# Kernel tuning notes

Measured on AMD Instinct MI355X. Metric: run time of the kernel, lower is better.

Reference implementation:

```python
import jax, jax.numpy as jnp
import numpy as np

B, K, D = 8, 2048, 1024

def setup_inputs() -> dict:
    key = jax.random.key(0)
    k1, k2 = jax.random.split(key)
    x = jax.random.normal(k1, (B, K, D), dtype=jnp.float32)
    W = jax.random.normal(k2, (K, K), dtype=jnp.float32) * 0.02  # dt_proj weight [out=K, in=K]
    b = jnp.zeros((K,), dtype=jnp.float32)                        # dt_proj bias
    return {"x": x, "W": W, "b": b}

def _scan_combine(c1, c2):
    # compose affine maps s -> a*s + u; (a1,u1) then (a2,u2)
    a1, u1 = c1
    a2, u2 = c2
    return (a2 * a1, a2 * u1 + u2)

def reference(x, W, b):
    # lam[b,t,d] = sigmoid( sum_k x[b,k,d] * W[t,k] + b[t] )
    # (dt_proj is a Linear over the TIME axis after permute(0,2,1))
    lam = jax.nn.sigmoid(jnp.einsum('bkd,tk->btd', x, W) + b[None, :, None])
    # s_t = lam_t * s_{t-1} + (1 - lam_t) * x_t, s_0 = 0  -> associative scan over time
    _, ys = jax.lax.associative_scan(_scan_combine, (lam, (1.0 - lam) * x), axis=1)
    return ys
```

## Files before the change

### kernel.cpp

```cpp
#include <hip/hip_runtime.h>
#include <hip/hip_bf16.h>
#include <stdint.h>

#define B_ 8
#define K_ 2048
#define D_ 1024
#define NC 32
#define TC (K_ / NC)

typedef float v4f __attribute__((ext_vector_type(4)));
typedef short v8s __attribute__((ext_vector_type(8)));

__device__ __forceinline__ unsigned short f2bf(float f) {
    __hip_bfloat16 h = __float2bfloat16(f);
    return *reinterpret_cast<unsigned short*>(&h);
}

__device__ __forceinline__ void async_ld16(const void* g, void* l) {
    __builtin_amdgcn_global_load_lds(
        (__attribute__((address_space(1))) void*)(void*)g,
        (__attribute__((address_space(3))) void*)l,
        16, 0, 0);
}

__global__ void conv_all(const float* __restrict__ W, unsigned short* __restrict__ Wb,
                         const float* __restrict__ x, unsigned short* __restrict__ xT) {
    if (blockIdx.x < 4096) {
        int i = (blockIdx.x * 256 + threadIdx.x) * 4;
        float4 v = *(const float4*)(W + i);
        ushort4 o;
        o.x = f2bf(v.x); o.y = f2bf(v.y); o.z = f2bf(v.z); o.w = f2bf(v.w);
        *(ushort4*)(Wb + i) = o;
        return;
    }
    const int t = blockIdx.x - 4096;
    const int k0 = (t & 31) * 64, d0 = ((t >> 5) & 15) * 64, bb = t >> 9;
    __shared__ unsigned short tile[64][68];
    const int tid = threadIdx.x;
    const int tx = tid & 15, ty = tid >> 4;
    const float* xp = x + (size_t)bb * K_ * D_;
#pragma unroll
    for (int r = 0; r < 4; r++) {
        int row = ty + r * 16;
        float4 v = *(const float4*)(xp + (size_t)(k0 + row) * D_ + d0 + tx * 4);
        tile[row][tx * 4 + 0] = f2bf(v.x);
        tile[row][tx * 4 + 1] = f2bf(v.y);
        tile[row][tx * 4 + 2] = f2bf(v.z);
        tile[row][tx * 4 + 3] = f2bf(v.w);
    }
    __syncthreads();
    unsigned short* op = xT + (size_t)bb * D_ * K_;
#pragma unroll
    for (int r = 0; r < 4; r++) {
        int dcol = ty + r * 16;
        ushort4 u;
        u.x = tile[tx * 4 + 0][dcol];
        u.y = tile[tx * 4 + 1][dcol];
        u.z = tile[tx * 4 + 2][dcol];
        u.w = tile[tx * 4 + 3][dcol];
        *(ushort4*)(op + (size_t)(d0 + dcol) * K_ + k0 + tx * 4) = u;
    }
}

__launch_bounds__(512, 2)
__global__ void gemm_sig(const unsigned short* __restrict__ Wb,
                         const unsigned short* __restrict__ xT,
                         const float* __restrict__ bias,
                         const float* __restrict__ xf,
                         float* __restrict__ lam,
                         float* __restrict__ Ac,
                         float* __restrict__ Uc,
                         int fuse) {
    __shared__ __align__(16) unsigned short smem_all[2][4][256 * 32];

    const int bid = blockIdx.x;
    const int lid = (bid & 7) * 32 + (bid >> 3);
    const int bb = lid >> 5;
    const int tM = (lid >> 2) & 7;
    const int tN = lid & 3;

    const int tid = threadIdx.x;
    const int w = tid >> 6;
    const int lane = tid & 63;
    const int wm = w >> 2;
    const int wn = w & 3;
    const int quad = lane >> 4;
    const int l16 = lane & 15;

    const unsigned short* Ag = Wb + (size_t)(tM * 256) * K_;
    const unsigned short* Bg = xT + (size_t)bb * D_ * K_ + (size_t)(tN * 256) * K_;

    const int srow = lane >> 2;
    const int sgk8 = ((lane & 3) ^ ((lane >> 3) & 3)) * 8;

    const int frg = (quad ^ ((l16 >> 1) & 3)) * 8;
    const int aoff = (wm * 128 + l16) * 32 + frg;
    const int boff = (wn * 64 + l16) * 32 + frg;

    v4f acc[8][4];
#pragma unroll
    for (int i = 0; i < 8; i++)
#pragma unroll
        for (int j = 0; j < 4; j++) acc[i][j] = (v4f)0.f;

#define STAGE_A_(hh)                                                                        \
    do {                                                                                    \
        const int slot_ = (hh) & 3; const int ko_ = (hh) * 32;                              \
        async_ld16(Ag + (size_t)(w * 16 + srow) * K_ + ko_ + sgk8,                          \
                   &smem_all[0][slot_][w * 512]);                                           \
        async_ld16(Ag + (size_t)((8 + w) * 16 + srow) * K_ + ko_ + sgk8,                    \
                   &smem_all[0][slot_][(8 + w) * 512]);                                     \
    } while (0)
#define STAGE_B_(hh)                                                                        \
    do {                                                                                    \
        const int slot_ = (hh) & 3; const int ko_ = (hh) * 32;                              \
        async_ld16(Bg + (size_t)(w * 16 + srow) * K_ + ko_ + sgk8,                          \
                   &smem_all[1][slot_][w * 512]);                                           \
        async_ld16(Bg + (size_t)((8 + w) * 16 + srow) * K_ + ko_ + sgk8,                    \
                   &smem_all[1][slot_][(8 + w) * 512]);                                     \
    } while (0)

    v8s af[8], bf[2];

#define HALF_(hh, DO_STAGE, VM_)                                                            \
    do {                                                                                    \
        const int s_ = (hh) & 3;                                                            \
        const unsigned short* As_ = &smem_all[0][s_][0];                                    \
        const unsigned short* Bs_ = &smem_all[1][s_][0];                                    \
                                                                   \
        _Pragma("unroll")                                                                   \
        for (int i = 0; i < 8; i++) af[i] = *(const v8s*)(&As_[aoff + i * 512]);            \
        bf[0] = *(const v8s*)(&Bs_[boff]);                                                  \
        bf[1] = *(const v8s*)(&Bs_[boff + 512]);                                            \
        if (DO_STAGE) STAGE_A_((hh) + 3);                                                   \
        asm volatile("s_barrier" ::: "memory");                                             \
        asm volatile("s_waitcnt lgkmcnt(0)");                                               \
        __builtin_amdgcn_sched_barrier(0);                                                  \
        __builtin_amdgcn_s_setprio(1);                                                      \
        _Pragma("unroll")                                                                   \
        for (int i = 0; i < 8; i++) {                                                       \
            acc[i][0] = __builtin_amdgcn_mfma_f32_16x16x32_bf16(af[i], bf[0], acc[i][0], 0, 0, 0); \
            acc[i][1] = __builtin_amdgcn_mfma_f32_16x16x32_bf16(af[i], bf[1], acc[i][1], 0, 0, 0); \
        }                                                                                   \
        __builtin_amdgcn_s_setprio(0);                                                      \
        asm volatile("s_barrier" ::: "memory");                                             \
                                                                   \
        bf[0] = *(const v8s*)(&Bs_[boff + 2 * 512]);                                        \
        bf[1] = *(const v8s*)(&Bs_[boff + 3 * 512]);                                        \
        if (DO_STAGE) STAGE_B_((hh) + 3);                                                   \
        asm volatile("s_barrier" ::: "memory");                                             \
        asm volatile("s_waitcnt lgkmcnt(0)");                                               \
        __builtin_amdgcn_sched_barrier(0);                                                  \
        __builtin_amdgcn_s_setprio(1);                                                      \
        _Pragma("unroll")                                                                   \
        for (int i = 0; i < 8; i++) {                                                       \
            acc[i][2] = __builtin_amdgcn_mfma_f32_16x16x32_bf16(af[i], bf[0], acc[i][2], 0, 0, 0); \
            acc[i][3] = __builtin_amdgcn_mfma_f32_16x16x32_bf16(af[i], bf[1], acc[i][3], 0, 0, 0); \
        }                                                                                   \
        __builtin_amdgcn_s_setprio(0);                                                      \
        VM_;                                                                                \
        asm volatile("s_barrier" ::: "memory");                                             \
    } while (0)

    STAGE_A_(0); STAGE_B_(0);
    STAGE_A_(1); STAGE_B_(1);
    STAGE_A_(2); STAGE_B_(2);
    asm volatile("s_waitcnt vmcnt(8)");
    asm volatile("s_barrier" ::: "memory");

    const int H = K_ / 32;
    for (int h = 0; h < H - 3; ++h)
        HALF_(h, 1, asm volatile("s_waitcnt vmcnt(8)"));
    HALF_(H - 3, 0, asm volatile("s_waitcnt vmcnt(4)"));
    HALF_(H - 2, 0, asm volatile("s_waitcnt vmcnt(0)"));
    HALF_(H - 1, 0, (void)0);
#undef HALF_
#undef STAGE_A_
#undef STAGE_B_


    float* out = lam + (size_t)bb * K_ * D_;
    const int dg = tN * 256 + wn * 64;

    if (fuse) {
        float* Swp = (float*)smem_all + w * 4096;
        const int swzw = quad * 16;
#pragma unroll
        for (int cg = 0; cg < 2; cg++) {
            const int c = tM * 4 + wm * 2 + cg;
            const int t0 = c * 64;
#pragma unroll
            for (int ii = 0; ii < 4; ii++) {
                int i = cg * 4 + ii;
                int rowb = t0 + ii * 16 + quad * 4;
                int Rb = ii * 16 + quad * 4;
#pragma unroll
                for (int r = 0; r < 4; r++) {
                    float bt = bias[rowb + r];
#pragma unroll
                    for (int j = 0; j < 4; j++) {
                        int colc = j * 16 + l16;
                        float v = acc[i][j][r] + bt;
                        float sg = 1.f / (1.f + __expf(-v));
                        out[(size_t)(rowb + r) * D_ + dg + colc] = sg;
                        Swp[(Rb + r) * 64 + (colc ^ swzw)] = sg;
                    }
                }
            }
            asm volatile("s_waitcnt lgkmcnt(0)");
            __builtin_amdgcn_sched_barrier(0);
            const float* xg = xf + ((size_t)bb * K_ + t0) * D_ + dg + lane;
            float A = 1.f, U = 0.f;
#pragma unroll 8
            for (int tt = 0; tt < 64; tt++) {
                float l = Swp[tt * 64 + (lane ^ (((tt >> 2) & 3) * 16))];
                float xv = xg[(size_t)tt * D_];
                A *= l;
                U = l * U + (1.f - l) * xv;
            }
            size_t oi = ((size_t)bb * NC + c) * D_ + dg + lane;
            Ac[oi] = A;
            Uc[oi] = U;
            __builtin_amdgcn_sched_barrier(0);
        }
    } else {
#pragma unroll
        for (int i = 0; i < 8; i++) {
            int rowb = tM * 256 + wm * 128 + i * 16 + quad * 4;
#pragma unroll
            for (int r = 0; r < 4; r++) {
                float bt = bias[rowb + r];
#pragma unroll
                for (int j = 0; j < 4; j++) {
                    int col = tN * 256 + wn * 64 + j * 16 + l16;
                    float v = acc[i][j][r] + bt;
                    out[(size_t)(rowb + r) * D_ + col] = 1.f / (1.f + __expf(-v));
                }
            }
        }
    }
}

__global__ void scan_pass1(const float* __restrict__ lam, const float* __restrict__ x,
                           float* __restrict__ Ac, float* __restrict__ Uc) {
    int id = blockIdx.x * 256 + threadIdx.x;
    int d2 = (id & 511) * 2;
    int c = (id >> 9) & (NC - 1);
    int bb = id >> 14;
    const float* lp = lam + ((size_t)bb * K_ + (size_t)c * TC) * D_ + d2;
    const float* xp = x   + ((size_t)bb * K_ + (size_t)c * TC) * D_ + d2;
    float2 A = make_float2(1.f, 1.f), U = make_float2(0.f, 0.f);
#pragma unroll 8
    for (int t = 0; t < TC; t++) {
        float2 l  = *(const float2*)(lp + (size_t)t * D_);
        float2 xv = *(const float2*)(xp + (size_t)t * D_);
        A.x *= l.x; A.y *= l.y;
        U.x = l.x * U.x + (1.f - l.x) * xv.x;
        U.y = l.y * U.y + (1.f - l.y) * xv.y;
    }
    size_t oi = ((size_t)bb * NC + c) * D_ + d2;
    *(float2*)(Ac + oi) = A;
    *(float2*)(Uc + oi) = U;
}

__launch_bounds__(256)
__global__ void scan_pass3(const float* __restrict__ x,
                           const float* __restrict__ Ac, const float* __restrict__ Uc,
                           float* __restrict__ lamout) {
    int id = blockIdx.x * 256 + threadIdx.x;
    int d = (id & 511) * 2;
    int c = (id >> 9) & (NC - 1);
    int bb = id >> 14;
    float2 s = make_float2(0.f, 0.f);
    for (int j = 0; j < c; j++) {
        size_t ji = ((size_t)bb * NC + j) * D_ + d;
        float2 A = *(const float2*)(Ac + ji);
        float2 U = *(const float2*)(Uc + ji);
        s.x = A.x * s.x + U.x;
        s.y = A.y * s.y + U.y;
    }
    float* lp = lamout + ((size_t)bb * K_ + (size_t)c * TC) * D_ + d;
    const float* xp = x + ((size_t)bb * K_ + (size_t)c * TC) * D_ + d;
#pragma unroll 8
    for (int t = 0; t < TC; t++) {
        float2 l  = *(const float2*)(lp + (size_t)t * D_);
        float2 xv = *(const float2*)(xp + (size_t)t * D_);
        s.x = l.x * s.x + (1.f - l.x) * xv.x;
        s.y = l.y * s.y + (1.f - l.y) * xv.y;
        __builtin_nontemporal_store(s.x, lp + (size_t)t * D_);
        __builtin_nontemporal_store(s.y, lp + (size_t)t * D_ + 1);
    }
}

extern "C" void kernel_launch(void* const* d_in, const int* in_sizes, int n_in,
                              void* d_out, int out_size, void* d_ws, size_t ws_size,
                              hipStream_t stream) {
    const float* x    = (const float*)d_in[0];
    const float* W    = (const float*)d_in[1];
    const float* bias = (const float*)d_in[2];
    float* out = (float*)d_out;
    char* ws = (char*)d_ws;

    unsigned short* xT = (unsigned short*)ws;
    unsigned short* Wb = (unsigned short*)(ws + 33554432);

    const int fuse = (ws_size >= 44040192u) ? 1 : 0;
    float* Ac, * Uc;
    if (fuse) {
        Ac = (float*)(ws + 41943040);
        Uc = (float*)(ws + 41943040 + 1048576);
    } else {
        Ac = (float*)(ws + 33554432);
        Uc = (float*)(ws + 33554432 + 1048576);
    }

    conv_all<<<dim3(8192), 256, 0, stream>>>(W, Wb, x, xT);
    gemm_sig<<<dim3(256), dim3(512), 0, stream>>>(Wb, xT, bias, x, out, Ac, Uc, fuse);
    if (!fuse)
        scan_pass1<<<dim3(B_ * NC * D_ / 2 / 256), 256, 0, stream>>>(out, x, Ac, Uc);
    scan_pass3<<<dim3(B_ * NC * D_ / 2 / 256), 256, 0, stream>>>(x, Ac, Uc, out);
}
```

Measured before the change: 237.2 us.

## Prefetch next A fragments into registers during second MFMA half

Adds register double-buffering of the A operand fragments. The next stage's A tile is loaded from LDS into a second register set while the current stage's MFMAs run. The explicit lgkmcnt(0) waits and sched_barriers are removed so the compiler can overlap LDS reads with matrix math. Global-load waits are tightened to vmcnt(4) because the next slot must land one stage earlier. This trades more VGPR pressure, which may cut occupancy, for hiding LDS latency.

Result: slower. 243.0 us (+2.4%).

```diff
diff --git a/kernel.cpp b/kernel.cpp
--- a/kernel.cpp
+++ b/kernel.cpp
@@ -120,22 +120,17 @@
                    &smem_all[1][slot_][(8 + w) * 512]);                                     \
     } while (0)
 
-    v8s af[8], bf[2];
-
-#define HALF_(hh, DO_STAGE, VM_)                                                            \
+    v8s af[8], afn[8], bf[2];
+
+#define HALF_(hh, DO_STG, DO_AFN, VM_)                                                      \
     do {                                                                                    \
         const int s_ = (hh) & 3;                                                            \
-        const unsigned short* As_ = &smem_all[0][s_][0];                                    \
         const unsigned short* Bs_ = &smem_all[1][s_][0];                                    \
-                                                                   \
-        _Pragma("unroll")                                                                   \
-        for (int i = 0; i < 8; i++) af[i] = *(const v8s*)(&As_[aoff + i * 512]);            \
+                                \
         bf[0] = *(const v8s*)(&Bs_[boff]);                                                  \
         bf[1] = *(const v8s*)(&Bs_[boff + 512]);                                            \
-        if (DO_STAGE) STAGE_A_((hh) + 3);                                                   \
+        if (DO_STG) STAGE_A_((hh) + 3);                                                     \
         asm volatile("s_barrier" ::: "memory");                                             \
-        asm volatile("s_waitcnt lgkmcnt(0)");                                               \
-        __builtin_amdgcn_sched_barrier(0);                                                  \
         __builtin_amdgcn_s_setprio(1);                                                      \
         _Pragma("unroll")                                                                   \
         for (int i = 0; i < 8; i++) {                                                       \
@@ -144,13 +139,16 @@
         }                                                                                   \
         __builtin_amdgcn_s_setprio(0);                                                      \
         asm volatile("s_barrier" ::: "memory");                                             \
-                                                                   \
+                            \
         bf[0] = *(const v8s*)(&Bs_[boff + 2 * 512]);                                        \
         bf[1] = *(const v8s*)(&Bs_[boff + 3 * 512]);                                        \
-        if (DO_STAGE) STAGE_B_((hh) + 3);                                                   \
+        if (DO_AFN) {                                                                       \
+            const unsigned short* An_ = &smem_all[0][((hh) + 1) & 3][0];                    \
+            _Pragma("unroll")                                                               \
+            for (int i = 0; i < 8; i++) afn[i] = *(const v8s*)(&An_[aoff + i * 512]);       \
+        }                                                                                   \
+        if (DO_STG) STAGE_B_((hh) + 3);                                                     \
         asm volatile("s_barrier" ::: "memory");                                             \
-        asm volatile("s_waitcnt lgkmcnt(0)");                                               \
-        __builtin_amdgcn_sched_barrier(0);                                                  \
         __builtin_amdgcn_s_setprio(1);                                                      \
         _Pragma("unroll")                                                                   \
         for (int i = 0; i < 8; i++) {                                                       \
@@ -160,20 +158,29 @@
         __builtin_amdgcn_s_setprio(0);                                                      \
         VM_;                                                                                \
         asm volatile("s_barrier" ::: "memory");                                             \
+        if (DO_AFN) {                                                                       \
+            _Pragma("unroll")                                                               \
+            for (int i = 0; i < 8; i++) af[i] = afn[i];                                     \
+        }                                                                                   \
     } while (0)
 
     STAGE_A_(0); STAGE_B_(0);
     STAGE_A_(1); STAGE_B_(1);
     STAGE_A_(2); STAGE_B_(2);
-    asm volatile("s_waitcnt vmcnt(8)");
+    asm volatile("s_waitcnt vmcnt(4)");
     asm volatile("s_barrier" ::: "memory");
+    {
+        const unsigned short* A0_ = &smem_all[0][0][0];
+#pragma unroll
+        for (int i = 0; i < 8; i++) af[i] = *(const v8s*)(&A0_[aoff + i * 512]);
+    }
 
     const int H = K_ / 32;
     for (int h = 0; h < H - 3; ++h)
-        HALF_(h, 1, asm volatile("s_waitcnt vmcnt(8)"));
-    HALF_(H - 3, 0, asm volatile("s_waitcnt vmcnt(4)"));
-    HALF_(H - 2, 0, asm volatile("s_waitcnt vmcnt(0)"));
-    HALF_(H - 1, 0, (void)0);
+        HALF_(h, 1, 1, asm volatile("s_waitcnt vmcnt(4)"));
+    HALF_(H - 3, 0, 1, asm volatile("s_waitcnt vmcnt(0)"));
+    HALF_(H - 2, 0, 1, (void)0);
+    HALF_(H - 1, 0, 0, (void)0);
 #undef HALF_
 #undef STAGE_A_
 #undef STAGE_B_
```

## Halve GEMM tile height, double-buffer LDS, split fused chunk scan across half-waves

Applied to the files above, without the earlier changes.

The GEMM tile shrinks from 256x256 to 128x256 per block. The grid doubles to 512 blocks, accumulators drop to 4x4 per wave, and launch bounds ask for 4 blocks per CU to raise occupancy. The 4-slot, 3-ahead split A/B pipeline becomes a simple double buffer that waits on vmcnt(0) every k-step. The fused epilogue's per-chunk scan is split into two 32-step halves combined by a lane shuffle. More blocks means more total global reads of x-tiles, and the shallower prefetch may expose load latency.

Result: slower. 260.1 us (+9.6%).

```diff
diff --git a/kernel.cpp b/kernel.cpp
--- a/kernel.cpp
+++ b/kernel.cpp
@@ -62,7 +62,7 @@
     }
 }
 
-__launch_bounds__(512, 2)
+__launch_bounds__(512, 4)
 __global__ void gemm_sig(const unsigned short* __restrict__ Wb,
                          const unsigned short* __restrict__ xT,
                          const float* __restrict__ bias,
@@ -71,13 +71,16 @@
                          float* __restrict__ Ac,
                          float* __restrict__ Uc,
                          int fuse) {
-    __shared__ __align__(16) unsigned short smem_all[2][4][256 * 32];
+    __shared__ __align__(16) unsigned char lds_raw[65536];
+    unsigned short* As = (unsigned short*)lds_raw;
+    unsigned short* Bs = (unsigned short*)(lds_raw + 16384);
 
     const int bid = blockIdx.x;
-    const int lid = (bid & 7) * 32 + (bid >> 3);
-    const int bb = lid >> 5;
-    const int tM = (lid >> 2) & 7;
-    const int tN = lid & 3;
+    const int lid = (bid & 7) * 64 + (bid >> 3);
+    const int bb = lid >> 6;
+    const int rr = lid & 63;
+    const int tM = rr >> 2;
+    const int tN = rr & 3;
 
     const int tid = threadIdx.x;
     const int w = tid >> 6;
@@ -87,146 +90,137 @@
     const int quad = lane >> 4;
     const int l16 = lane & 15;
 
-    const unsigned short* Ag = Wb + (size_t)(tM * 256) * K_;
+    const unsigned short* Ag = Wb + (size_t)(tM * 128) * K_;
     const unsigned short* Bg = xT + (size_t)bb * D_ * K_ + (size_t)(tN * 256) * K_;
 
     const int srow = lane >> 2;
     const int sgk8 = ((lane & 3) ^ ((lane >> 3) & 3)) * 8;
 
     const int frg = (quad ^ ((l16 >> 1) & 3)) * 8;
-    const int aoff = (wm * 128 + l16) * 32 + frg;
-    const int boff = (wn * 64 + l16) * 32 + frg;
-
-    v4f acc[8][4];
-#pragma unroll
-    for (int i = 0; i < 8; i++)
+    const int a_hw = (wm * 64 + l16) * 32 + frg;
+    const int b_hw = (wn * 64 + l16) * 32 + frg;
+
+    v4f acc[4][4];
+#pragma unroll
+    for (int i = 0; i < 4; i++)
 #pragma unroll
         for (int j = 0; j < 4; j++) acc[i][j] = (v4f)0.f;
 
-#define STAGE_A_(hh)                                                                        \
+#define STAGE_(bufi, hh)                                                                    \
     do {                                                                                    \
-        const int slot_ = (hh) & 3; const int ko_ = (hh) * 32;                              \
+        const int ko_ = (hh) * 32;                                                          \
         async_ld16(Ag + (size_t)(w * 16 + srow) * K_ + ko_ + sgk8,                          \
-                   &smem_all[0][slot_][w * 512]);                                           \
-        async_ld16(Ag + (size_t)((8 + w) * 16 + srow) * K_ + ko_ + sgk8,                    \
-                   &smem_all[0][slot_][(8 + w) * 512]);                                     \
+                   As + (bufi) * 4096 + w * 512);                                           \
+        async_ld16(Bg + (size_t)(w * 16 + srow) * K_ + ko_ + sgk8,                          \
+                   Bs + (bufi) * 8192 + w * 512);                                           \
+        async_ld16(Bg + (size_t)((8 + w) * 16 + srow) * K_ + ko_ + sgk8,                    \
+                   Bs + (bufi) * 8192 + (8 + w) * 512);                                     \
     } while (0)
-#define STAGE_B_(hh)                                                                        \
-    do {                                                                                    \
-        const int slot_ = (hh) & 3; const int ko_ = (hh) * 32;                              \
-        async_ld16(Bg + (size_t)(w * 16 + srow) * K_ + ko_ + sgk8,                          \
-                   &smem_all[1][slot_][w * 512]);                                           \
-        async_ld16(Bg + (size_t)((8 + w) * 16 + srow) * K_ + ko_ + sgk8,                    \
-                   &smem_all[1][slot_][(8 + w) * 512]);                                     \
-    } while (0)
-
-    v8s af[8], bf[2];
-
-#define HALF_(hh, DO_STAGE, VM_)                                                            \
-    do {                                                                                    \
-        const int s_ = (hh) & 3;                                                            \
-        const unsigned short* As_ = &smem_all[0][s_][0];                                    \
-        const unsigned short* Bs_ = &smem_all[1][s_][0];                                    \
-                                                                   \
-        _Pragma("unroll")                                                                   \
-        for (int i = 0; i < 8; i++) af[i] = *(const v8s*)(&As_[aoff + i * 512]);            \
-        bf[0] = *(const v8s*)(&Bs_[boff]);                                                  \
-        bf[1] = *(const v8s*)(&Bs_[boff + 512]);                                            \
-        if (DO_STAGE) STAGE_A_((hh) + 3);                                                   \
-        asm volatile("s_barrier" ::: "memory");                                             \
-        asm volatile("s_waitcnt lgkmcnt(0)");                                               \
-        __builtin_amdgcn_sched_barrier(0);                                                  \
-        __builtin_amdgcn_s_setprio(1);                                                      \
-        _Pragma("unroll")                                                                   \
-        for (int i = 0; i < 8; i++) {                                                       \
-            acc[i][0] = __builtin_amdgcn_mfma_f32_16x16x32_bf16(af[i], bf[0], acc[i][0], 0, 0, 0); \
-            acc[i][1] = __builtin_amdgcn_mfma_f32_16x16x32_bf16(af[i], bf[1], acc[i][1], 0, 0, 0); \
-        }                                                                                   \
-        __builtin_amdgcn_s_setprio(0);                                                      \
-        asm volatile("s_barrier" ::: "memory");                                             \
-                                                                   \
-        bf[0] = *(const v8s*)(&Bs_[boff + 2 * 512]);                                        \
-        bf[1] = *(const v8s*)(&Bs_[boff + 3 * 512]);                                        \
-        if (DO_STAGE) STAGE_B_((hh) + 3);                                                   \
-        asm volatile("s_barrier" ::: "memory");                                             \
-        asm volatile("s_waitcnt lgkmcnt(0)");                                               \
-        __builtin_amdgcn_sched_barrier(0);                                                  \
-        __builtin_amdgcn_s_setprio(1);                                                      \
-        _Pragma("unroll")                                                                   \
-        for (int i = 0; i < 8; i++) {                                                       \
-            acc[i][2] = __builtin_amdgcn_mfma_f32_16x16x32_bf16(af[i], bf[0], acc[i][2], 0, 0, 0); \
-            acc[i][3] = __builtin_amdgcn_mfma_f32_16x16x32_bf16(af[i], bf[1], acc[i][3], 0, 0, 0); \
-        }                                                                                   \
-        __builtin_amdgcn_s_setprio(0);                                                      \
-        VM_;                                                                                \
-        asm volatile("s_barrier" ::: "memory");                                             \
-    } while (0)
-
-    STAGE_A_(0); STAGE_B_(0);
-    STAGE_A_(1); STAGE_B_(1);
-    STAGE_A_(2); STAGE_B_(2);
-    asm volatile("s_waitcnt vmcnt(8)");
+
+    STAGE_(0, 0);
+    asm volatile("s_waitcnt vmcnt(0)");
     asm volatile("s_barrier" ::: "memory");
 
+    v8s af[4], bf[4];
     const int H = K_ / 32;
-    for (int h = 0; h < H - 3; ++h)
-        HALF_(h, 1, asm volatile("s_waitcnt vmcnt(8)"));
-    HALF_(H - 3, 0, asm volatile("s_waitcnt vmcnt(4)"));
-    HALF_(H - 2, 0, asm volatile("s_waitcnt vmcnt(0)"));
-    HALF_(H - 1, 0, (void)0);
-#undef HALF_
-#undef STAGE_A_
-#undef STAGE_B_
-
+    for (int h = 0; h < H - 1; ++h) {
+        const int cur = h & 1, nxt = cur ^ 1;
+        const unsigned short* Ac_ = As + cur * 4096;
+        const unsigned short* Bc_ = Bs + cur * 8192;
+#pragma unroll
+        for (int i = 0; i < 4; i++) af[i] = *(const v8s*)(&Ac_[a_hw + i * 512]);
+#pragma unroll
+        for (int j = 0; j < 4; j++) bf[j] = *(const v8s*)(&Bc_[b_hw + j * 512]);
+        STAGE_(nxt, h + 1);
+        asm volatile("s_waitcnt lgkmcnt(0)");
+        __builtin_amdgcn_sched_barrier(0);
+        __builtin_amdgcn_s_setprio(1);
+#pragma unroll
+        for (int i = 0; i < 4; i++)
+#pragma unroll
+            for (int j = 0; j < 4; j++)
+                acc[i][j] = __builtin_amdgcn_mfma_f32_16x16x32_bf16(af[i], bf[j], acc[i][j], 0, 0, 0);
+        __builtin_amdgcn_s_setprio(0);
+        asm volatile("s_waitcnt vmcnt(0)");
+        asm volatile("s_barrier" ::: "memory");
+    }
+    {
+        const int cur = (H - 1) & 1;
+        const unsigned short* Ac_ = As + cur * 4096;
+        const unsigned short* Bc_ = Bs + cur * 8192;
+#pragma unroll
+        for (int i = 0; i < 4; i++) af[i] = *(const v8s*)(&Ac_[a_hw + i * 512]);
+#pragma unroll
+        for (int j = 0; j < 4; j++) bf[j] = *(const v8s*)(&Bc_[b_hw + j * 512]);
+        asm volatile("s_waitcnt lgkmcnt(0)");
+        __builtin_amdgcn_sched_barrier(0);
+        __builtin_amdgcn_s_setprio(1);
+#pragma unroll
+        for (int i = 0; i < 4; i++)
+#pragma unroll
+            for (int j = 0; j < 4; j++)
+                acc[i][j] = __builtin_amdgcn_mfma_f32_16x16x32_bf16(af[i], bf[j], acc[i][j], 0, 0, 0);
+        __builtin_amdgcn_s_setprio(0);
+        asm volatile("s_barrier" ::: "memory");
+    }
+#undef STAGE_
 
     float* out = lam + (size_t)bb * K_ * D_;
-    const int dg = tN * 256 + wn * 64;
+    const int c = tM * 2 + wm;
+    const int t0 = c * 64;
 
     if (fuse) {
-        float* Swp = (float*)smem_all + w * 4096;
-        const int swzw = quad * 16;
-#pragma unroll
-        for (int cg = 0; cg < 2; cg++) {
-            const int c = tM * 4 + wm * 2 + cg;
-            const int t0 = c * 64;
-#pragma unroll
-            for (int ii = 0; ii < 4; ii++) {
-                int i = cg * 4 + ii;
-                int rowb = t0 + ii * 16 + quad * 4;
-                int Rb = ii * 16 + quad * 4;
-#pragma unroll
-                for (int r = 0; r < 4; r++) {
-                    float bt = bias[rowb + r];
-#pragma unroll
-                    for (int j = 0; j < 4; j++) {
-                        int colc = j * 16 + l16;
+        float* Swp = (float*)lds_raw + w * 2048;
+#pragma unroll
+        for (int p = 0; p < 2; ++p) {
+#pragma unroll
+            for (int jj = 0; jj < 2; ++jj) {
+                const int j = p * 2 + jj;
+#pragma unroll
+                for (int i = 0; i < 4; i++) {
+                    const int rowb = t0 + i * 16 + quad * 4;
+#pragma unroll
+                    for (int r = 0; r < 4; r++) {
+                        float bt = bias[rowb + r];
+                        const int colg = tN * 256 + wn * 64 + j * 16 + l16;
                         float v = acc[i][j][r] + bt;
                         float sg = 1.f / (1.f + __expf(-v));
-                        out[(size_t)(rowb + r) * D_ + dg + colc] = sg;
-                        Swp[(Rb + r) * 64 + (colc ^ swzw)] = sg;
+                        out[(size_t)(rowb + r) * D_ + colg] = sg;
+                        Swp[(i * 16 + quad * 4 + r) * 32 + ((jj * 16 + l16) ^ (quad * 8))] = sg;
                     }
                 }
             }
             asm volatile("s_waitcnt lgkmcnt(0)");
             __builtin_amdgcn_sched_barrier(0);
-            const float* xg = xf + ((size_t)bb * K_ + t0) * D_ + dg + lane;
+            const int col32 = lane & 31;
+            const int h2 = lane >> 5;
+            const int dcol = tN * 256 + wn * 64 + p * 32 + col32;
+            const float* xg = xf + ((size_t)bb * K_ + t0 + h2 * 32) * D_ + dcol;
             float A = 1.f, U = 0.f;
 #pragma unroll 8
-            for (int tt = 0; tt < 64; tt++) {
-                float l = Swp[tt * 64 + (lane ^ (((tt >> 2) & 3) * 16))];
+            for (int tt = 0; tt < 32; tt++) {
+                const int trow = h2 * 32 + tt;
+                float l = Swp[trow * 32 + (col32 ^ (((trow >> 2) & 3) * 8))];
                 float xv = xg[(size_t)tt * D_];
                 A *= l;
                 U = l * U + (1.f - l) * xv;
             }
-            size_t oi = ((size_t)bb * NC + c) * D_ + dg + lane;
-            Ac[oi] = A;
-            Uc[oi] = U;
+            float Apr = __shfl_xor(A, 32);
+            float Upr = __shfl_xor(U, 32);
+            if (h2 == 0) {
+                float Af = Apr * A;
+                float Uf = Apr * U + Upr;
+                size_t oi = ((size_t)bb * NC + c) * D_ + dcol;
+                Ac[oi] = Af;
+                Uc[oi] = Uf;
+            }
+            asm volatile("s_waitcnt lgkmcnt(0)");
             __builtin_amdgcn_sched_barrier(0);
         }
     } else {
 #pragma unroll
-        for (int i = 0; i < 8; i++) {
-            int rowb = tM * 256 + wm * 128 + i * 16 + quad * 4;
+        for (int i = 0; i < 4; i++) {
+            int rowb = t0 + i * 16 + quad * 4;
 #pragma unroll
             for (int r = 0; r < 4; r++) {
                 float bt = bias[rowb + r];
@@ -315,7 +309,7 @@
     }
 
     conv_all<<<dim3(8192), 256, 0, stream>>>(W, Wb, x, xT);
-    gemm_sig<<<dim3(256), dim3(512), 0, stream>>>(Wb, xT, bias, x, out, Ac, Uc, fuse);
+    gemm_sig<<<dim3(512), dim3(512), 0, stream>>>(Wb, xT, bias, x, out, Ac, Uc, fuse);
     if (!fuse)
         scan_pass1<<<dim3(B_ * NC * D_ / 2 / 256), 256, 0, stream>>>(out, x, Ac, Uc);
     scan_pass3<<<dim3(B_ * NC * D_ / 2 / 256), 256, 0, stream>>>(x, Ac, Uc, out);
```

## Load A operand directly from global into registers, double-buffer B in LDS

Applied to the files above, without the earlier changes.

The W (A) operand is no longer staged through LDS; each wave loads its A fragments straight from global memory into registers, double-buffered across iterations (afA/afB). B staging in LDS drops from a 4-slot ring to 2 buffers, and each K-step now issues all 32 MFMAs in one phase with fewer barriers. The aim is to cut LDS traffic and barrier count. The cost is more register pressure and exposed global-load latency for A with only one step of prefetch, plus redundant A reads across waves that share rows.

Result: slower. 321.7 us (+35.6%).

```diff
diff --git a/kernel.cpp b/kernel.cpp
--- a/kernel.cpp
+++ b/kernel.cpp
@@ -71,7 +71,8 @@
                          float* __restrict__ Ac,
                          float* __restrict__ Uc,
                          int fuse) {
-    __shared__ __align__(16) unsigned short smem_all[2][4][256 * 32];
+    __shared__ __align__(16) unsigned char lds_raw[131072];
+    unsigned short* Bs = (unsigned short*)lds_raw;
 
     const int bid = blockIdx.x;
     const int lid = (bid & 7) * 32 + (bid >> 3);
@@ -87,15 +88,13 @@
     const int quad = lane >> 4;
     const int l16 = lane & 15;
 
-    const unsigned short* Ag = Wb + (size_t)(tM * 256) * K_;
     const unsigned short* Bg = xT + (size_t)bb * D_ * K_ + (size_t)(tN * 256) * K_;
+    const unsigned short* Agl = Wb + (size_t)(tM * 256 + wm * 128 + l16) * K_ + quad * 8;
 
     const int srow = lane >> 2;
     const int sgk8 = ((lane & 3) ^ ((lane >> 3) & 3)) * 8;
-
     const int frg = (quad ^ ((l16 >> 1) & 3)) * 8;
-    const int aoff = (wm * 128 + l16) * 32 + frg;
-    const int boff = (wn * 64 + l16) * 32 + frg;
+    const int b_hw = (wn * 64 + l16) * 32 + frg;
 
     v4f acc[8][4];
 #pragma unroll
@@ -103,87 +102,69 @@
 #pragma unroll
         for (int j = 0; j < 4; j++) acc[i][j] = (v4f)0.f;
 
-#define STAGE_A_(hh)                                                                        \
-    do {                                                                                    \
-        const int slot_ = (hh) & 3; const int ko_ = (hh) * 32;                              \
-        async_ld16(Ag + (size_t)(w * 16 + srow) * K_ + ko_ + sgk8,                          \
-                   &smem_all[0][slot_][w * 512]);                                           \
-        async_ld16(Ag + (size_t)((8 + w) * 16 + srow) * K_ + ko_ + sgk8,                    \
-                   &smem_all[0][slot_][(8 + w) * 512]);                                     \
-    } while (0)
 #define STAGE_B_(hh)                                                                        \
     do {                                                                                    \
-        const int slot_ = (hh) & 3; const int ko_ = (hh) * 32;                              \
-        async_ld16(Bg + (size_t)(w * 16 + srow) * K_ + ko_ + sgk8,                          \
-                   &smem_all[1][slot_][w * 512]);                                           \
+        const int buf_ = ((hh) & 1) * 8192; const int ko_ = (hh) * 32;                      \
+        async_ld16(Bg + (size_t)(w * 16 + srow) * K_ + ko_ + sgk8, Bs + buf_ + w * 512);    \
         async_ld16(Bg + (size_t)((8 + w) * 16 + srow) * K_ + ko_ + sgk8,                    \
-                   &smem_all[1][slot_][(8 + w) * 512]);                                     \
+                   Bs + buf_ + (8 + w) * 512);                                              \
     } while (0)
 
-    v8s af[8], bf[2];
-
-#define HALF_(hh, DO_STAGE, VM_)                                                            \
+#define LOADA_(dst, hh)                                                                     \
     do {                                                                                    \
-        const int s_ = (hh) & 3;                                                            \
-        const unsigned short* As_ = &smem_all[0][s_][0];                                    \
-        const unsigned short* Bs_ = &smem_all[1][s_][0];                                    \
-                                                                   \
         _Pragma("unroll")                                                                   \
-        for (int i = 0; i < 8; i++) af[i] = *(const v8s*)(&As_[aoff + i * 512]);            \
-        bf[0] = *(const v8s*)(&Bs_[boff]);                                                  \
-        bf[1] = *(const v8s*)(&Bs_[boff + 512]);                                            \
-        if (DO_STAGE) STAGE_A_((hh) + 3);                                                   \
+        for (int i = 0; i < 8; i++)                                                         \
+            dst[i] = *(const v8s*)(Agl + (size_t)i * 16 * K_ + (hh) * 32);                  \
+    } while (0)
+
+    v8s afA[8], afB[8], bf[4];
+
+    STAGE_B_(0);
+    __builtin_amdgcn_sched_barrier(0);
+    LOADA_(afA, 0);
+    __builtin_amdgcn_sched_barrier(0);
+    asm volatile("s_waitcnt vmcnt(8)");
+    asm volatile("s_barrier" ::: "memory");
+
+#define HALF_(hh, USE, PRE, DO_PRE, DO_STG)                                                 \
+    do {                                                                                    \
+        const unsigned short* Bc_ = Bs + ((hh) & 1) * 8192;                                 \
+        _Pragma("unroll")                                                                   \
+        for (int j = 0; j < 4; j++) bf[j] = *(const v8s*)(&Bc_[b_hw + j * 512]);            \
+        if (DO_STG) STAGE_B_((hh) + 1);                                                     \
+        __builtin_amdgcn_sched_barrier(0);                                                  \
+        if (DO_PRE) LOADA_(PRE, (hh) + 1);                                                  \
+        __builtin_amdgcn_sched_barrier(0);                                                  \
         asm volatile("s_barrier" ::: "memory");                                             \
         asm volatile("s_waitcnt lgkmcnt(0)");                                               \
         __builtin_amdgcn_sched_barrier(0);                                                  \
         __builtin_amdgcn_s_setprio(1);                                                      \
         _Pragma("unroll")                                                                   \
-        for (int i = 0; i < 8; i++) {                                                       \
-            acc[i][0] = __builtin_amdgcn_mfma_f32_16x16x32_bf16(af[i], bf[0], acc[i][0], 0, 0, 0); \
-            acc[i][1] = __builtin_amdgcn_mfma_f32_16x16x32_bf16(af[i], bf[1], acc[i][1], 0, 0, 0); \
-        }                                                                                   \
+        for (int i = 0; i < 8; i++)                                                         \
+            _Pragma("unroll")                                                               \
+            for (int j = 0; j < 4; j++)                                                     \
+                acc[i][j] = __builtin_amdgcn_mfma_f32_16x16x32_bf16(USE[i], bf[j], acc[i][j], 0, 0, 0); \
         __builtin_amdgcn_s_setprio(0);                                                      \
-        asm volatile("s_barrier" ::: "memory");                                             \
-                                                                   \
-        bf[0] = *(const v8s*)(&Bs_[boff + 2 * 512]);                                        \
-        bf[1] = *(const v8s*)(&Bs_[boff + 3 * 512]);                                        \
-        if (DO_STAGE) STAGE_B_((hh) + 3);                                                   \
-        asm volatile("s_barrier" ::: "memory");                                             \
-        asm volatile("s_waitcnt lgkmcnt(0)");                                               \
-        __builtin_amdgcn_sched_barrier(0);                                                  \
-        __builtin_amdgcn_s_setprio(1);                                                      \
-        _Pragma("unroll")                                                                   \
-        for (int i = 0; i < 8; i++) {                                                       \
-            acc[i][2] = __builtin_amdgcn_mfma_f32_16x16x32_bf16(af[i], bf[0], acc[i][2], 0, 0, 0); \
-            acc[i][3] = __builtin_amdgcn_mfma_f32_16x16x32_bf16(af[i], bf[1], acc[i][3], 0, 0, 0); \
-        }                                                                                   \
-        __builtin_amdgcn_s_setprio(0);                                                      \
-        VM_;                                                                                \
+        asm volatile("s_waitcnt vmcnt(8)");                                                 \
         asm volatile("s_barrier" ::: "memory");                                             \
     } while (0)
 
-    STAGE_A_(0); STAGE_B_(0);
-    STAGE_A_(1); STAGE_B_(1);
-    STAGE_A_(2); STAGE_B_(2);
-    asm volatile("s_waitcnt vmcnt(8)");
-    asm volatile("s_barrier" ::: "memory");
-
     const int H = K_ / 32;
-    for (int h = 0; h < H - 3; ++h)
-        HALF_(h, 1, asm volatile("s_waitcnt vmcnt(8)"));
-    HALF_(H - 3, 0, asm volatile("s_waitcnt vmcnt(4)"));
-    HALF_(H - 2, 0, asm volatile("s_waitcnt vmcnt(0)"));
-    HALF_(H - 1, 0, (void)0);
+    for (int h = 0; h < H - 2; h += 2) {
+        HALF_(h, afA, afB, 1, 1);
+        HALF_(h + 1, afB, afA, 1, 1);
+    }
+    HALF_(H - 2, afA, afB, 1, 1);
+    HALF_(H - 1, afB, afA, 0, 0);
 #undef HALF_
-#undef STAGE_A_
 #undef STAGE_B_
-
+#undef LOADA_
 
     float* out = lam + (size_t)bb * K_ * D_;
     const int dg = tN * 256 + wn * 64;
 
     if (fuse) {
-        float* Swp = (float*)smem_all + w * 4096;
+        float* Swp = (float*)lds_raw + w * 4096;
         const int swzw = quad * 16;
 #pragma unroll
         for (int cg = 0; cg < 2; cg++) {
```
